# Kernel optimization log

Hardware: AMD Instinct MI355X
Metric: run time of the kernel (lower is better)

## Reference

```python
import jax, jax.numpy as jnp
import numpy as np

MAX_NORM = 1.0 - 1e-5  # Poincare ball (c=1) boundary clip, geoopt-style
NUM_HEADS = 8

def _norm(x):
    return jnp.sqrt(jnp.sum(x * x, axis=-1, keepdims=True) + 1e-30)

def projx(x):
    n = _norm(x)
    return jnp.where(n > MAX_NORM, x * (MAX_NORM / n), x)

def expmap0(u):
    n = _norm(u)
    return jnp.tanh(n) * u / n

def logmap0(x):
    n = _norm(x)
    return jnp.arctanh(jnp.minimum(n, MAX_NORM)) * x / n

def mobius_add(x, y):
    xy = jnp.sum(x * y, axis=-1, keepdims=True)
    x2 = jnp.sum(x * x, axis=-1, keepdims=True)
    y2 = jnp.sum(y * y, axis=-1, keepdims=True)
    num = (1.0 + 2.0 * xy + y2) * x + (1.0 - x2) * y
    den = 1.0 + 2.0 * xy + x2 * y2
    return num / jnp.maximum(den, 1e-15)

def mobius_matvec(M, x):
    xn = _norm(x)
    mx = x @ M.T
    mxn = _norm(mx)
    return jnp.tanh(mxn / xn * jnp.arctanh(jnp.minimum(xn, MAX_NORM))) * mx / mxn

def man_linear(x, W, b):
    # Manifold_Linear: mobius matvec + mobius bias add + project (geoopt MobiusLinear)
    return projx(mobius_add(mobius_matvec(W, x), b))

def mob_relu(x):
    # Mob_Act(ReLU): act in tangent space at origin
    return projx(expmap0(jax.nn.relu(logmap0(x))))

def layer_norm(x, g, b):
    mu = jnp.mean(x, axis=-1, keepdims=True)
    v = jnp.var(x, axis=-1, keepdims=True)
    return (x - mu) / jnp.sqrt(v + 1e-5) * g + b

def mha_tan_space(x_q, x_kv, Wq, bq, Wk, bk, Wv, bv, Wo, bo, num_heads):
    # ManifoldMHA with att_metric='tan_space': manifold linear projections,
    # scaled dot-product attention in the tangent space at the origin.
    q = logmap0(man_linear(x_q, Wq, bq))   # (S, B, E)
    k = logmap0(man_linear(x_kv, Wk, bk))  # (T, B, E)
    v = logmap0(man_linear(x_kv, Wv, bv))  # (T, B, E)
    S, B, E = q.shape
    hd = E // num_heads
    def split(t):  # (T,B,E) -> (B,H,T,hd)
        return t.reshape(t.shape[0], B, num_heads, hd).transpose(1, 2, 0, 3)
    qh, kh, vh = split(q), split(k), split(v)
    scores = jnp.einsum('bhqd,bhkd->bhqk', qh, kh) / np.sqrt(hd).astype(np.float32)
    attn = jax.nn.softmax(scores, axis=-1)
    o = jnp.einsum('bhqk,bhkd->bhqd', attn, vh)  # (B,H,S,hd)
    o = o.transpose(2, 0, 1, 3).reshape(S, B, E)
    o = expmap0(o)
    return man_linear(o, Wo, bo)

def forward_block(x, ln1_g, ln1_b, ln2_g, ln2_b, Wq, bq, Wk, bk, Wv, bv, Wo, bo, W1, b1, W2, b2):
    residual = x
    h = expmap0(layer_norm(logmap0(x), ln1_g, ln1_b))
    h = mha_tan_space(h, h, Wq, bq, Wk, bk, Wv, bv, Wo, bo, NUM_HEADS)
    h = projx(h)
    h = projx(mobius_add(h, residual))
    residual = h
    h = projx(expmap0(layer_norm(logmap0(h), ln2_g, ln2_b)))
    h = mob_relu(man_linear(h, W1, b1))   # fc1 = Manifold_Linear + Mob_Act
    h = projx(h)                          # act_dropout (identity, eval) + projx
    h = mob_relu(man_linear(h, W2, b2))   # fc2
    h = projx(mobius_add(h, residual))
    return h

def setup_inputs() -> dict:
    key = jax.random.key(0)
    ks = jax.random.split(key, 18)
    S, B, E, F = 128, 256, 512, 2048
    sE = 1.0 / np.sqrt(E)
    sF = 1.0 / np.sqrt(F)
    # input points must lie inside the unit ball: randn scaled small
    x = jax.random.normal(ks[0], (S, B, E), jnp.float32) * 0.02
    def w(k, o, i, s):
        return jax.random.normal(k, (o, i), jnp.float32) * s
    def bias(k, d):
        return jax.random.normal(k, (d,), jnp.float32) * 1e-3
    return {
        'x': x,
        'ln1_g': jnp.ones((E,), jnp.float32), 'ln1_b': jnp.zeros((E,), jnp.float32),
        'ln2_g': jnp.ones((E,), jnp.float32), 'ln2_b': jnp.zeros((E,), jnp.float32),
        'Wq': w(ks[1], E, E, sE), 'bq': bias(ks[2], E),
        'Wk': w(ks[3], E, E, sE), 'bk': bias(ks[4], E),
        'Wv': w(ks[5], E, E, sE), 'bv': bias(ks[6], E),
        'Wo': w(ks[7], E, E, sE), 'bo': bias(ks[8], E),
        'W1': w(ks[9], F, E, sE), 'b1': bias(ks[10], F),
        'W2': w(ks[11], E, F, sF), 'b2': bias(ks[12], E),
    }

def reference(x, ln1_g, ln1_b, ln2_g, ln2_b, Wq, bq, Wk, bk, Wv, bv, Wo, bo, W1, b1, W2, b2):
    return forward_block(x, ln1_g, ln1_b, ln2_g, ln2_b, Wq, bq, Wk, bk, Wv, bv, Wo, bo, W1, b1, W2, b2)
```

## Files before the change

kernel.cpp:

```cpp
#include <hip/hip_runtime.h>
#include <math.h>

#define S_DIM 128
#define B_DIM 256
#define E_DIM 512
#define F_DIM 2048
#define N_ROWS (S_DIM * B_DIM)
#define CH 8192
#define MAXN 0.99999f

typedef __bf16 bf16x8 __attribute__((ext_vector_type(8)));
typedef float f32x4 __attribute__((ext_vector_type(4)));

__device__ __forceinline__ float frcp(float x) { return __builtin_amdgcn_rcpf(x); }
__device__ __forceinline__ float frsq(float x) { return __builtin_amdgcn_rsqf(x); }
__device__ __forceinline__ float fexp2(float x) { return __builtin_amdgcn_exp2f(x); }
__device__ __forceinline__ float flog2(float x) { return __builtin_amdgcn_logf(x); }
__device__ __forceinline__ float fatanh(float x) {
  return 0.34657359f * flog2((1.f + x) * frcp(1.f - x));
}
__device__ __forceinline__ float ftanh(float x) {
  float t = fexp2(x * -2.88539008f);
  return (1.f - t) * frcp(1.f + t);
}

__device__ __forceinline__ ushort f2bf(float f) {
  __bf16 h = (__bf16)f;
  return __builtin_bit_cast(ushort, h);
}
__device__ __forceinline__ uint pack2(float a, float b) {
  return (uint)f2bf(a) | ((uint)f2bf(b) << 16);
}

__device__ __forceinline__ void gld16(const ushort* g, ushort* l) {
  __builtin_amdgcn_global_load_lds(
      (const __attribute__((address_space(1))) void*)g,
      (__attribute__((address_space(3))) void*)l, 16, 0, 0);
}

template <int K>
__device__ __forceinline__ void waveRed(float (&v)[K]) {
#pragma unroll
  for (int o = 1; o < 64; o <<= 1) {
#pragma unroll
    for (int i = 0; i < K; ++i) v[i] += __shfl_xor(v[i], o);
  }
}

__global__ __launch_bounds__(256) void k_f2bf(const float* __restrict__ in,
                                              ushort* __restrict__ out, int n) {
  for (int i = blockIdx.x * 256 + threadIdx.x; i < n; i += gridDim.x * 256)
    out[i] = f2bf(in[i]);
}

__global__ void k_bsums(const float* __restrict__ bq, const float* __restrict__ bk,
                        const float* __restrict__ bv, const float* __restrict__ g1,
                        const float* __restrict__ lb1, float* __restrict__ bs) {
  int lane = threadIdx.x;
  float p[6];
#pragma unroll
  for (int i = 0; i < 6; ++i) p[i] = 0.f;
  for (int i = lane; i < E_DIM; i += 64) {
    float a = bq[i]; p[0] += a * a;
    a = bk[i]; p[1] += a * a;
    a = bv[i]; p[2] += a * a;
    float g = g1[i], l = lb1[i];
    p[3] += g * g; p[4] += g * l; p[5] += l * l;
  }
  waveRed<6>(p);
  if (lane == 0) {
    bs[0] = p[0]; bs[1] = p[1]; bs[2] = p[2];
    bs[7] = p[3]; bs[8] = p[4]; bs[9] = p[5];
  }
}

__global__ __launch_bounds__(256) void k_stage1(
    const float* __restrict__ x, const float* __restrict__ g,
    const float* __restrict__ bb, const float* __restrict__ bs,
    ushort* __restrict__ h, float* __restrict__ hn) {
  int wv = threadIdx.x >> 6, lane = threadIdx.x & 63;
  int row = blockIdx.x * 8 + wv * 2;
  size_t base = (size_t)row * E_DIM + lane * 8;
  float v[2][8], gv[8], bv[8];
  *(float4*)&v[0][0] = *(const float4*)(x + base);
  *(float4*)&v[0][4] = *(const float4*)(x + base + 4);
  *(float4*)&v[1][0] = *(const float4*)(x + base + E_DIM);
  *(float4*)&v[1][4] = *(const float4*)(x + base + E_DIM + 4);
  *(float4*)&gv[0] = *(const float4*)(g + lane * 8);
  *(float4*)&gv[4] = *(const float4*)(g + lane * 8 + 4);
  *(float4*)&bv[0] = *(const float4*)(bb + lane * 8);
  *(float4*)&bv[4] = *(const float4*)(bb + lane * 8 + 4);
  float s[10];
#pragma unroll
  for (int i = 0; i < 10; ++i) s[i] = 0.f;
#pragma unroll
  for (int i = 0; i < 8; ++i) {
    float gg = gv[i] * gv[i], gb = gv[i] * bv[i];
#pragma unroll
    for (int r2 = 0; r2 < 2; ++r2) {
      float vv = v[r2][i];
      s[r2 * 5 + 0] += vv * vv;
      s[r2 * 5 + 1] += vv;
      s[r2 * 5 + 2] += vv * vv * gg;
      s[r2 * 5 + 3] += vv * gg;
      s[r2 * 5 + 4] += vv * gb;
    }
  }
  waveRed<10>(s);
  float Sg2 = bs[7], Sgb = bs[8], Sb2 = bs[9];
#pragma unroll
  for (int r2 = 0; r2 < 2; ++r2) {
    float T0 = s[r2 * 5 + 0], T1 = s[r2 * 5 + 1], T2 = s[r2 * 5 + 2];
    float T3 = s[r2 * 5 + 3], T4 = s[r2 * 5 + 4];
    float se = T0 + 1e-30f;
    float rn = frsq(se);
    float n = se * rn;
    float a = fatanh(fminf(n, MAXN)) * rn;
    float mu = a * T1 * (1.f / 512.f);
    float var = fmaxf(a * a * T0 * (1.f / 512.f) - mu * mu, 0.f);
    float rstd = frsq(var + 1e-5f);
    float A = a * rstd, B = -mu * rstd;
    float se2 = fmaxf(A * A * T2 + 2.f * A * B * T3 + 2.f * A * T4 +
                          B * B * Sg2 + 2.f * B * Sgb + Sb2, 0.f) + 1e-30f;
    float rn2 = frsq(se2);
    float n2 = se2 * rn2;
    float th = ftanh(n2);
    float f = th * rn2;
    float e[8];
#pragma unroll
    for (int i = 0; i < 8; ++i) e[i] = (A * v[r2][i] + B) * gv[i] + bv[i];
    uint4 o = {pack2(e[0] * f, e[1] * f), pack2(e[2] * f, e[3] * f),
               pack2(e[4] * f, e[5] * f), pack2(e[6] * f, e[7] * f)};
    *reinterpret_cast<uint4*>(h + base + r2 * E_DIM) = o;
    if (lane == 0) hn[row + r2] = th;
  }
}

__global__ __launch_bounds__(256) void k_qkv_fused(
    const ushort* __restrict__ A, const ushort* __restrict__ B,
    const float* __restrict__ xn_arr, const float* __restrict__ bias,
    const float* __restrict__ bs_sb2, ushort* __restrict__ qout) {
  __shared__ __align__(16) ushort As[32 * 32];
  __shared__ __align__(16) ushort Bs[512 * 32];
  __shared__ float redu[2][32][4];
  __shared__ float coefA[32], coefB[32];
  const int K = E_DIM;
  int tid = threadIdx.x;
  int w = tid >> 6, lane = tid & 63;
  int r0 = blockIdx.x * 32;

  const ushort* gA =
      A + ((size_t)r0 + (w & 1) * 16 + (lane >> 2)) * K + (lane & 3) * 8;
  ushort* lA = As + ((w & 1) * 16) * 32;
  const ushort* gB = B + ((size_t)w * 128 + (lane >> 2)) * K + (lane & 3) * 8;
  ushort* lB = Bs + (w * 128) * 32;

  int fro = (lane & 15) * 32 + (lane >> 4) * 8;
  const ushort* raA = As + fro;
  const ushort* raB = Bs + w * 128 * 32 + fro;

  f32x4 zero = {0.f, 0.f, 0.f, 0.f};
  f32x4 acc[2][8];
#pragma unroll
  for (int i = 0; i < 2; ++i)
#pragma unroll
    for (int j = 0; j < 8; ++j) acc[i][j] = zero;

  for (int kt = 0; kt < K; kt += 32) {
    __syncthreads();
    if (w < 2) gld16(gA + kt, lA);
#pragma unroll
    for (int i = 0; i < 8; ++i)
      gld16(gB + kt + (size_t)i * 16 * K, lB + i * 16 * 32);
    __syncthreads();
    bf16x8 af[2], bfv[8];
    af[0] = *reinterpret_cast<const bf16x8*>(raA);
    af[1] = *reinterpret_cast<const bf16x8*>(raA + 512);
#pragma unroll
    for (int j = 0; j < 8; ++j)
      bfv[j] = *reinterpret_cast<const bf16x8*>(raB + j * 512);
#pragma unroll
    for (int i = 0; i < 2; ++i)
#pragma unroll
      for (int j = 0; j < 8; ++j)
        acc[i][j] = __builtin_amdgcn_mfma_f32_16x16x32_bf16(af[i], bfv[j],
                                                            acc[i][j], 0, 0, 0);
  }

  float bvv[8];
#pragma unroll
  for (int j = 0; j < 8; ++j) bvv[j] = bias[w * 128 + j * 16 + (lane & 15)];
#pragma unroll
  for (int ti = 0; ti < 2; ++ti) {
#pragma unroll
    for (int reg = 0; reg < 4; ++reg) {
      float p2 = 0.f, pb = 0.f;
#pragma unroll
      for (int j = 0; j < 8; ++j) {
        float c = acc[ti][j][reg];
        p2 += c * c;
        pb += c * bvv[j];
      }
#pragma unroll
      for (int o = 1; o < 16; o <<= 1) {
        p2 += __shfl_xor(p2, o);
        pb += __shfl_xor(pb, o);
      }
      if ((lane & 15) == 0) {
        int row = ti * 16 + (lane >> 4) * 4 + reg;
        redu[0][row][w] = p2;
        redu[1][row][w] = pb;
      }
    }
  }
  __syncthreads();
  if (tid < 32) {
    int row = tid;
    float S0 = (redu[0][row][0] + redu[0][row][1]) +
               (redu[0][row][2] + redu[0][row][3]);
    float S1 = (redu[1][row][0] + redu[1][row][1]) +
               (redu[1][row][2] + redu[1][row][3]);
    float S2 = *bs_sb2;
    float se = S0 + 1e-30f;
    float rmx = frsq(se);
    float mxn = se * rmx;
    float xn = xn_arr[r0 + row];
    float aa = fatanh(fminf(xn, MAXN));
    float tt = ftanh(mxn * frcp(xn) * aa);
    float c = tt * rmx;
    float xy = c * S1, y2 = S2, x2 = tt * tt;
    float c1 = 1.f + 2.f * xy + y2, c2 = 1.f - x2;
    float iden = frcp(fmaxf(1.f + 2.f * xy + x2 * y2, 1e-15f));
    float cc1 = c1 * c * iden, cc2 = c2 * iden;
    float un2 =
        fmaxf(cc1 * cc1 * S0 + 2.f * cc1 * cc2 * S1 + cc2 * cc2 * S2, 0.f);
    float ue = un2 + 1e-30f;
    float run = frsq(ue);
    float un = ue * run;
    float ne = fminf(un, MAXN);
    float f = fatanh(ne) * run;
    coefA[row] = cc1 * f;
    coefB[row] = cc2 * f;
  }
  __syncthreads();
#pragma unroll
  for (int ti = 0; ti < 2; ++ti) {
#pragma unroll
    for (int reg = 0; reg < 4; ++reg) {
      int row = ti * 16 + (lane >> 4) * 4 + reg;
      float cA = coefA[row], cB = coefB[row];
      ushort* orow = qout + (size_t)(r0 + row) * E_DIM + w * 128 + (lane & 15);
#pragma unroll
      for (int j = 0; j < 8; ++j)
        orow[j * 16] = f2bf(cA * acc[ti][j][reg] + cB * bvv[j]);
    }
  }
}

__global__ __launch_bounds__(256) void k_gemm_bf16(
    const ushort* __restrict__ A, const ushort* __restrict__ B,
    float* __restrict__ C, int K, int M, int kseg,
    unsigned long long partStride) {
  __shared__ __align__(16) ushort As[128 * 32];
  __shared__ __align__(16) ushort Bs[128 * 32];
  int tid = threadIdx.x;
  int w = tid >> 6, lane = tid & 63;
  int wm = w >> 1, wn = w & 1;
  size_t row0 = (size_t)blockIdx.y * 128;
  size_t col0 = (size_t)blockIdx.x * 128;
  int k0 = blockIdx.z * kseg;

  const ushort* gA =
      A + (row0 + w * 32 + (lane >> 2)) * (size_t)K + (lane & 3) * 8 + k0;
  const ushort* gB =
      B + (col0 + w * 32 + (lane >> 2)) * (size_t)K + (lane & 3) * 8 + k0;
  ushort* lA = As + (w * 32) * 32;
  ushort* lB = Bs + (w * 32) * 32;
  const int rowK16 = 16 * K;

  int fro = (lane & 15) * 32 + (lane >> 4) * 8;
  const ushort* raA = As + (wm * 64) * 32 + fro;
  const ushort* raB = Bs + (wn * 64) * 32 + fro;

  f32x4 zero = {0.f, 0.f, 0.f, 0.f};
  f32x4 acc[4][4];
#pragma unroll
  for (int i = 0; i < 4; ++i)
#pragma unroll
    for (int j = 0; j < 4; ++j) acc[i][j] = zero;

  for (int kt = 0; kt < kseg; kt += 32) {
    __syncthreads();
    gld16(gA + kt, lA);
    gld16(gA + kt + rowK16, lA + 16 * 32);
    gld16(gB + kt, lB);
    gld16(gB + kt + rowK16, lB + 16 * 32);
    __syncthreads();
    bf16x8 af[4], bfv[4];
#pragma unroll
    for (int t = 0; t < 4; ++t) {
      af[t] = *reinterpret_cast<const bf16x8*>(raA + t * 512);
      bfv[t] = *reinterpret_cast<const bf16x8*>(raB + t * 512);
    }
#pragma unroll
    for (int i = 0; i < 4; ++i)
#pragma unroll
      for (int j = 0; j < 4; ++j)
        acc[i][j] = __builtin_amdgcn_mfma_f32_16x16x32_bf16(af[i], bfv[j],
                                                            acc[i][j], 0, 0, 0);
  }
  float* Cz = C + (size_t)blockIdx.z * partStride;
  int crow = wm * 64 + (lane >> 4) * 4;
  int ccol = (int)col0 + wn * 64 + (lane & 15);
#pragma unroll
  for (int ti = 0; ti < 4; ++ti) {
    size_t r = row0 + crow + ti * 16;
#pragma unroll
    for (int tj = 0; tj < 4; ++tj) {
      int cc = ccol + tj * 16;
#pragma unroll
      for (int reg = 0; reg < 4; ++reg)
        Cz[(r + reg) * (size_t)M + cc] = acc[ti][tj][reg];
    }
  }
}

__global__ __launch_bounds__(256) void k_attn(const ushort* __restrict__ q,
                                              const ushort* __restrict__ k,
                                              const ushort* __restrict__ v,
                                              float* __restrict__ o) {
  __shared__ __align__(16) ushort smem[27136];
  ushort* Qs = smem;
  ushort* Ks = smem + 9216;
  ushort* VTs = smem + 18432;
  ushort* Ps = smem;
  int bh = blockIdx.x;
  int b = bh >> 3, h = bh & 7;
  int tid = threadIdx.x;
  int w = tid >> 6, lane = tid & 63;
  const size_t BE = (size_t)B_DIM * E_DIM;
  size_t gbase = (size_t)b * E_DIM + (size_t)h * 64;

  {
    int s = tid >> 1, half = (tid & 1) * 32;
    const ushort* qr = q + gbase + (size_t)s * BE + half;
    const ushort* kr = k + gbase + (size_t)s * BE + half;
    const ushort* vr = v + gbase + (size_t)s * BE + half;
#pragma unroll
    for (int j = 0; j < 4; ++j) {
      *reinterpret_cast<uint4*>(&Qs[s * 72 + half + j * 8]) =
          *reinterpret_cast<const uint4*>(qr + j * 8);
      *reinterpret_cast<uint4*>(&Ks[s * 72 + half + j * 8]) =
          *reinterpret_cast<const uint4*>(kr + j * 8);
    }
    ushort tv[32];
#pragma unroll
    for (int j = 0; j < 4; ++j)
      *reinterpret_cast<uint4*>(&tv[j * 8]) =
          *reinterpret_cast<const uint4*>(vr + j * 8);
#pragma unroll
    for (int d = 0; d < 32; ++d) VTs[(half + d) * 136 + s] = tv[d];
  }
  __syncthreads();

  f32x4 zero = {0.f, 0.f, 0.f, 0.f};
  f32x4 sacc[2][8];
#pragma unroll
  for (int i = 0; i < 2; ++i)
#pragma unroll
    for (int j = 0; j < 8; ++j) sacc[i][j] = zero;
  {
    const ushort* qb = Qs + (w * 32 + (lane & 15)) * 72 + (lane >> 4) * 8;
    const ushort* kb = Ks + (lane & 15) * 72 + (lane >> 4) * 8;
#pragma unroll
    for (int kk = 0; kk < 2; ++kk) {
      bf16x8 a0 = *reinterpret_cast<const bf16x8*>(qb + kk * 32);
      bf16x8 a1 = *reinterpret_cast<const bf16x8*>(qb + 16 * 72 + kk * 32);
#pragma unroll
      for (int tj = 0; tj < 8; ++tj) {
        bf16x8 bf = *reinterpret_cast<const bf16x8*>(kb + tj * 16 * 72 + kk * 32);
        sacc[0][tj] = __builtin_amdgcn_mfma_f32_16x16x32_bf16(a0, bf,
                                                              sacc[0][tj], 0, 0, 0);
        sacc[1][tj] = __builtin_amdgcn_mfma_f32_16x16x32_bf16(a1, bf,
                                                              sacc[1][tj], 0, 0, 0);
      }
    }
  }

#pragma unroll
  for (int ti = 0; ti < 2; ++ti) {
#pragma unroll
    for (int r = 0; r < 4; ++r) {
      float mx = -1e30f;
#pragma unroll
      for (int tj = 0; tj < 8; ++tj) mx = fmaxf(mx, sacc[ti][tj][r]);
      mx = fmaxf(mx, __shfl_xor(mx, 1));
      mx = fmaxf(mx, __shfl_xor(mx, 2));
      mx = fmaxf(mx, __shfl_xor(mx, 4));
      mx = fmaxf(mx, __shfl_xor(mx, 8));
      float l = 0.f;
#pragma unroll
      for (int tj = 0; tj < 8; ++tj) {
        float e = fexp2((sacc[ti][tj][r] - mx) * (0.125f * 1.44269504f));
        sacc[ti][tj][r] = e;
        l += e;
      }
      l += __shfl_xor(l, 1);
      l += __shfl_xor(l, 2);
      l += __shfl_xor(l, 4);
      l += __shfl_xor(l, 8);
      float inv = frcp(l);
#pragma unroll
      for (int tj = 0; tj < 8; ++tj) sacc[ti][tj][r] *= inv;
    }
  }

  __syncthreads();
  {
    int qr0 = w * 32 + (lane >> 4) * 4;
    int kc = lane & 15;
#pragma unroll
    for (int ti = 0; ti < 2; ++ti)
#pragma unroll
      for (int tj = 0; tj < 8; ++tj)
#pragma unroll
        for (int r = 0; r < 4; ++r)
          Ps[(qr0 + ti * 16 + r) * 136 + tj * 16 + kc] =
              f2bf(sacc[ti][tj][r]);
  }
  __syncthreads();

  f32x4 oacc[2][4];
#pragma unroll
  for (int i = 0; i < 2; ++i)
#pragma unroll
    for (int j = 0; j < 4; ++j) oacc[i][j] = zero;
  {
    const ushort* pb = Ps + (w * 32 + (lane & 15)) * 136 + (lane >> 4) * 8;
    const ushort* vb = VTs + (lane & 15) * 136 + (lane >> 4) * 8;
#pragma unroll
    for (int kk = 0; kk < 4; ++kk) {
      bf16x8 a0 = *reinterpret_cast<const bf16x8*>(pb + kk * 32);
      bf16x8 a1 = *reinterpret_cast<const bf16x8*>(pb + 16 * 136 + kk * 32);
#pragma unroll
      for (int tj = 0; tj < 4; ++tj) {
        bf16x8 bv = *reinterpret_cast<const bf16x8*>(vb + tj * 16 * 136 + kk * 32);
        oacc[0][tj] = __builtin_amdgcn_mfma_f32_16x16x32_bf16(a0, bv,
                                                              oacc[0][tj], 0, 0, 0);
        oacc[1][tj] = __builtin_amdgcn_mfma_f32_16x16x32_bf16(a1, bv,
                                                              oacc[1][tj], 0, 0, 0);
      }
    }
  }

  {
    int qr0 = w * 32 + (lane >> 4) * 4;
    int dc = lane & 15;
#pragma unroll
    for (int ti = 0; ti < 2; ++ti)
#pragma unroll
      for (int tj = 0; tj < 4; ++tj)
#pragma unroll
        for (int r = 0; r < 4; ++r)
          o[(size_t)(qr0 + ti * 16 + r) * BE + gbase + tj * 16 + dc] =
              oacc[ti][tj][r];
  }
}

__global__ __launch_bounds__(256) void k_expmap_rows(const float* __restrict__ in,
                                                     ushort* __restrict__ out,
                                                     float* __restrict__ nrm) {
  int wv = threadIdx.x >> 6, lane = threadIdx.x & 63;
  int row = blockIdx.x * 8 + wv * 2;
  size_t base = (size_t)row * E_DIM + lane * 8;
  float v[2][8];
  *(float4*)&v[0][0] = *(const float4*)(in + base);
  *(float4*)&v[0][4] = *(const float4*)(in + base + 4);
  *(float4*)&v[1][0] = *(const float4*)(in + base + E_DIM);
  *(float4*)&v[1][4] = *(const float4*)(in + base + E_DIM + 4);
  float s[2] = {0.f, 0.f};
#pragma unroll
  for (int i = 0; i < 8; ++i) {
    s[0] += v[0][i] * v[0][i];
    s[1] += v[1][i] * v[1][i];
  }
  waveRed<2>(s);
#pragma unroll
  for (int r2 = 0; r2 < 2; ++r2) {
    float se = s[r2] + 1e-30f;
    float rn = frsq(se);
    float n = se * rn;
    float th = ftanh(n);
    float f = th * rn;
    uint4 o = {pack2(v[r2][0] * f, v[r2][1] * f), pack2(v[r2][2] * f, v[r2][3] * f),
               pack2(v[r2][4] * f, v[r2][5] * f), pack2(v[r2][6] * f, v[r2][7] * f)};
    *reinterpret_cast<uint4*>(out + base + r2 * E_DIM) = o;
    if (lane == 0) nrm[row + r2] = th;
  }
}

__global__ __launch_bounds__(256) void k_epi_attnout(
    float* __restrict__ mo, const float* __restrict__ xn_arr,
    const float* __restrict__ bo, const float* __restrict__ xin,
    const float* __restrict__ g2, const float* __restrict__ b2,
    ushort* __restrict__ h2, float* __restrict__ h2n) {
  int row = blockIdx.x * 4 + (threadIdx.x >> 6);
  int lane = threadIdx.x & 63;
  size_t base = (size_t)row * E_DIM + lane * 8;
  float m[8], bv[8];
  *(float4*)&m[0] = *(const float4*)(mo + base);
  *(float4*)&m[4] = *(const float4*)(mo + base + 4);
  *(float4*)&bv[0] = *(const float4*)(bo + lane * 8);
  *(float4*)&bv[4] = *(const float4*)(bo + lane * 8 + 4);
  float s[5] = {0.f, 0.f, 0.f, 0.f, 0.f};
#pragma unroll
  for (int i = 0; i < 8; ++i) {
    s[0] += m[i] * m[i]; s[1] += m[i] * bv[i]; s[2] += bv[i] * bv[i];
    s[3] += m[i]; s[4] += bv[i];
  }
  waveRed<5>(s);
  float se = s[0] + 1e-30f;
  float rmx = frsq(se);
  float mxn = se * rmx;
  float xn = xn_arr[row];
  float aa = fatanh(fminf(xn, MAXN));
  float tt = ftanh(mxn * frcp(xn) * aa);
  float c = tt * rmx;
  float xy = c * s[1], y2 = s[2], x2 = tt * tt;
  float c1 = 1.f + 2.f * xy + y2, c2 = 1.f - x2;
  float iden = frcp(fmaxf(1.f + 2.f * xy + x2 * y2, 1e-15f));
  float cc1 = c1 * c * iden, cc2 = c2 * iden;
  float un2 = fmaxf(cc1 * cc1 * s[0] + 2.f * cc1 * cc2 * s[1] + cc2 * cc2 * s[2], 0.f);
  float ue = un2 + 1e-30f;
  float run = frsq(ue);
  float un = ue * run;
  float ps = un > MAXN ? MAXN * run : 1.f;
  float zn = fminf(un, MAXN);
  float z[8];
#pragma unroll
  for (int i = 0; i < 8; ++i) z[i] = (cc1 * m[i] + cc2 * bv[i]) * ps;
  float sumz = ps * (cc1 * s[3] + cc2 * s[4]);
  float r[8];
  *(float4*)&r[0] = *(const float4*)(xin + base);
  *(float4*)&r[4] = *(const float4*)(xin + base + 4);
  float t2[3] = {0.f, 0.f, 0.f};
#pragma unroll
  for (int i = 0; i < 8; ++i) {
    t2[0] += z[i] * r[i]; t2[1] += r[i] * r[i]; t2[2] += r[i];
  }
  waveRed<3>(t2);
  float xy2 = t2[0], y22 = t2[1], x22 = zn * zn;
  float d1 = 1.f + 2.f * xy2 + y22, d2 = 1.f - x22;
  float iden2 = frcp(fmaxf(1.f + 2.f * xy2 + x22 * y22, 1e-15f));
  float wn2 = fmaxf(iden2 * iden2 *
                        (d1 * d1 * x22 + 2.f * d1 * d2 * xy2 + d2 * d2 * y22),
                    0.f);
  float we = wn2 + 1e-30f;
  float rwn = frsq(we);
  float wn = we * rwn;
  float ps2 = wn > MAXN ? MAXN * rwn : 1.f;
  float w[8];
#pragma unroll
  for (int i = 0; i < 8; ++i) w[i] = (d1 * z[i] + d2 * r[i]) * iden2 * ps2;
  *(float4*)(mo + base) = *(float4*)&w[0];
  *(float4*)(mo + base + 4) = *(float4*)&w[4];
  float ne = fminf(wn, MAXN);
  float ath = fatanh(ne);
  float lf = ath * frcp(ne);
  float sumw = ps2 * iden2 * (d1 * sumz + d2 * t2[2]);
  float mu = lf * sumw * (1.f / 512.f);
  float var = fmaxf(ath * ath * (1.f / 512.f) - mu * mu, 0.f);
  float rstd = frsq(var + 1e-5f);
  float gv[8], b2v[8];
  *(float4*)&gv[0] = *(const float4*)(g2 + lane * 8);
  *(float4*)&gv[4] = *(const float4*)(g2 + lane * 8 + 4);
  *(float4*)&b2v[0] = *(const float4*)(b2 + lane * 8);
  *(float4*)&b2v[4] = *(const float4*)(b2 + lane * 8 + 4);
  float e[8];
  float s3[1] = {0.f};
#pragma unroll
  for (int i = 0; i < 8; ++i) {
    e[i] = (lf * w[i] - mu) * rstd * gv[i] + b2v[i];
    s3[0] += e[i] * e[i];
  }
  waveRed<1>(s3);
  float s3e = s3[0] + 1e-30f;
  float rn3 = frsq(s3e);
  float n3 = s3e * rn3;
  float en = ftanh(n3);
  float f = en * rn3;
  if (en > MAXN) f *= MAXN * frcp(en);
  uint4 o = {pack2(e[0] * f, e[1] * f), pack2(e[2] * f, e[3] * f),
             pack2(e[4] * f, e[5] * f), pack2(e[6] * f, e[7] * f)};
  *reinterpret_cast<uint4*>(h2 + base) = o;
  if (lane == 0) h2n[row] = fminf(en, MAXN);
}

__global__ __launch_bounds__(256) void k_epi_ffn1(const float* __restrict__ mr_,
                                                  const float* __restrict__ xn_arr,
                                                  const float* __restrict__ bias,
                                                  ushort* __restrict__ hid,
                                                  float* __restrict__ hn_out) {
  int wv = threadIdx.x >> 6, lane = threadIdx.x & 63;
  int row = blockIdx.x * 8 + wv * 2;
  const float* mr = mr_ + (size_t)row * F_DIM + lane * 32;
  const float* br = bias + lane * 32;
  float m[2][32], bv[32];
#pragma unroll
  for (int j = 0; j < 8; ++j) {
    *(float4*)&m[0][j * 4] = *(const float4*)(mr + j * 4);
    *(float4*)&m[1][j * 4] = *(const float4*)(mr + F_DIM + j * 4);
    *(float4*)&bv[j * 4] = *(const float4*)(br + j * 4);
  }
  float s[5];
#pragma unroll
  for (int i = 0; i < 5; ++i) s[i] = 0.f;
#pragma unroll
  for (int i = 0; i < 32; ++i) {
#pragma unroll
    for (int r2 = 0; r2 < 2; ++r2) {
      s[r2 * 2 + 0] += m[r2][i] * m[r2][i];
      s[r2 * 2 + 1] += m[r2][i] * bv[i];
    }
    s[4] += bv[i] * bv[i];
  }
  waveRed<5>(s);
  float s2[2] = {0.f, 0.f};
#pragma unroll
  for (int r2 = 0; r2 < 2; ++r2) {
    float S0 = s[r2 * 2 + 0], S1 = s[r2 * 2 + 1], S2 = s[4];
    float se = S0 + 1e-30f;
    float rmx = frsq(se);
    float mxn = se * rmx;
    float xn = xn_arr[row + r2];
    float aa = fatanh(fminf(xn, MAXN));
    float tt = ftanh(mxn * frcp(xn) * aa);
    float c = tt * rmx;
    float xy = c * S1, y2 = S2, x2 = tt * tt;
    float c1 = 1.f + 2.f * xy + y2, c2 = 1.f - x2;
    float iden = frcp(fmaxf(1.f + 2.f * xy + x2 * y2, 1e-15f));
    float cc1 = c1 * c * iden, cc2 = c2 * iden;
    float un2 = fmaxf(cc1 * cc1 * S0 + 2.f * cc1 * cc2 * S1 + cc2 * cc2 * S2, 0.f);
    float ue = un2 + 1e-30f;
    float run = frsq(ue);
    float un = ue * run;
    float zn = fminf(un, MAXN);
    float lf = fatanh(zn) * run;
#pragma unroll
    for (int i = 0; i < 32; ++i) {
      m[r2][i] = fmaxf((cc1 * m[r2][i] + cc2 * bv[i]) * lf, 0.f);
      s2[r2] += m[r2][i] * m[r2][i];
    }
  }
  waveRed<2>(s2);
#pragma unroll
  for (int r2 = 0; r2 < 2; ++r2) {
    float s2e = s2[r2] + 1e-30f;
    float rrn = frsq(s2e);
    float rn = s2e * rrn;
    float en = ftanh(rn);
    float f = en * rrn;
    if (en > MAXN) f *= MAXN * frcp(en);
    ushort* hr = hid + (size_t)(row + r2) * F_DIM + lane * 32;
#pragma unroll
    for (int j = 0; j < 4; ++j) {
      uint4 o = {pack2(m[r2][j * 8 + 0] * f, m[r2][j * 8 + 1] * f),
                 pack2(m[r2][j * 8 + 2] * f, m[r2][j * 8 + 3] * f),
                 pack2(m[r2][j * 8 + 4] * f, m[r2][j * 8 + 5] * f),
                 pack2(m[r2][j * 8 + 6] * f, m[r2][j * 8 + 7] * f)};
      *reinterpret_cast<uint4*>(hr + j * 8) = o;
    }
    if (lane == 0) hn_out[row + r2] = fminf(en, MAXN);
  }
}

__global__ __launch_bounds__(256) void k_epi_final(
    const float* __restrict__ m2, const float* __restrict__ xn_arr,
    const float* __restrict__ bias, const float* __restrict__ res,
    float* __restrict__ out) {
  int wv = threadIdx.x >> 6, lane = threadIdx.x & 63;
  int row = blockIdx.x * 8 + wv * 2;
  size_t base = (size_t)row * E_DIM + lane * 8;
  const size_t P2 = (size_t)CH * E_DIM;
  float m[2][8], bv[8], q[2][8];
#pragma unroll
  for (int r2 = 0; r2 < 2; ++r2) {
    float ta[8], tb[8];
    *(float4*)&ta[0] = *(const float4*)(m2 + base + r2 * E_DIM);
    *(float4*)&ta[4] = *(const float4*)(m2 + base + r2 * E_DIM + 4);
    *(float4*)&tb[0] = *(const float4*)(m2 + P2 + base + r2 * E_DIM);
    *(float4*)&tb[4] = *(const float4*)(m2 + P2 + base + r2 * E_DIM + 4);
#pragma unroll
    for (int i = 0; i < 8; ++i) m[r2][i] = ta[i] + tb[i];
    *(float4*)&q[r2][0] = *(const float4*)(res + base + r2 * E_DIM);
    *(float4*)&q[r2][4] = *(const float4*)(res + base + r2 * E_DIM + 4);
  }
  *(float4*)&bv[0] = *(const float4*)(bias + lane * 8);
  *(float4*)&bv[4] = *(const float4*)(bias + lane * 8 + 4);
  float s[7];
#pragma unroll
  for (int i = 0; i < 7; ++i) s[i] = 0.f;
#pragma unroll
  for (int i = 0; i < 8; ++i) {
#pragma unroll
    for (int r2 = 0; r2 < 2; ++r2) {
      s[r2 * 3 + 0] += m[r2][i] * m[r2][i];
      s[r2 * 3 + 1] += m[r2][i] * bv[i];
      s[r2 * 3 + 2] += q[r2][i] * q[r2][i];
    }
    s[6] += bv[i] * bv[i];
  }
  waveRed<7>(s);
  float r[2][8];
  float s2[4];
#pragma unroll
  for (int i = 0; i < 4; ++i) s2[i] = 0.f;
#pragma unroll
  for (int r2 = 0; r2 < 2; ++r2) {
    float S0 = s[r2 * 3 + 0], S1 = s[r2 * 3 + 1], S2 = s[6];
    float se = S0 + 1e-30f;
    float rmx = frsq(se);
    float mxn = se * rmx;
    float xn = xn_arr[row + r2];
    float aa = fatanh(fminf(xn, MAXN));
    float tt = ftanh(mxn * frcp(xn) * aa);
    float c = tt * rmx;
    float xy = c * S1, y2 = S2, x2 = tt * tt;
    float c1 = 1.f + 2.f * xy + y2, c2 = 1.f - x2;
    float iden = frcp(fmaxf(1.f + 2.f * xy + x2 * y2, 1e-15f));
    float cc1 = c1 * c * iden, cc2 = c2 * iden;
    float un2 = fmaxf(cc1 * cc1 * S0 + 2.f * cc1 * cc2 * S1 + cc2 * cc2 * S2, 0.f);
    float ue = un2 + 1e-30f;
    float run = frsq(ue);
    float un = ue * run;
    float zn = fminf(un, MAXN);
    float lf = fatanh(zn) * run;
#pragma unroll
    for (int i = 0; i < 8; ++i) {
      r[r2][i] = fmaxf((cc1 * m[r2][i] + cc2 * bv[i]) * lf, 0.f);
      s2[r2 * 2 + 0] += r[r2][i] * r[r2][i];
      s2[r2 * 2 + 1] += r[r2][i] * q[r2][i];
    }
  }
  waveRed<4>(s2);
#pragma unroll
  for (int r2 = 0; r2 < 2; ++r2) {
    float s2e = s2[r2 * 2 + 0] + 1e-30f;
    float rrn = frsq(s2e);
    float rn = s2e * rrn;
    float en = ftanh(rn);
    float f = en * rrn;
    if (en > MAXN) f *= MAXN * frcp(en);
    float hn = fminf(en, MAXN);
    float xy2 = f * s2[r2 * 2 + 1], y22 = s[r2 * 3 + 2], x22 = hn * hn;
    float d1 = 1.f + 2.f * xy2 + y22, d2 = 1.f - x22;
    float iden2 = frcp(fmaxf(1.f + 2.f * xy2 + x22 * y22, 1e-15f));
    float wn2 = fmaxf(iden2 * iden2 *
                          (d1 * d1 * x22 + 2.f * d1 * d2 * xy2 + d2 * d2 * y22),
                      0.f);
    float we = wn2 + 1e-30f;
    float rwn = frsq(we);
    float wn = we * rwn;
    float ps2 = wn > MAXN ? MAXN * rwn : 1.f;
    float w[8];
#pragma unroll
    for (int i = 0; i < 8; ++i)
      w[i] = (d1 * r[r2][i] * f + d2 * q[r2][i]) * iden2 * ps2;
    *(float4*)(out + base + r2 * E_DIM) = *(float4*)&w[0];
    *(float4*)(out + base + r2 * E_DIM + 4) = *(float4*)&w[4];
  }
}

extern "C" void kernel_launch(void* const* d_in, const int* in_sizes, int n_in,
                              void* d_out, int out_size, void* d_ws,
                              size_t ws_size, hipStream_t stream) {
  const float* x   = (const float*)d_in[0];
  const float* g1  = (const float*)d_in[1];
  const float* lb1 = (const float*)d_in[2];
  const float* g2  = (const float*)d_in[3];
  const float* lb2 = (const float*)d_in[4];
  const float* Wq  = (const float*)d_in[5];
  const float* bq  = (const float*)d_in[6];
  const float* Wk  = (const float*)d_in[7];
  const float* bk  = (const float*)d_in[8];
  const float* Wv  = (const float*)d_in[9];
  const float* bv  = (const float*)d_in[10];
  const float* Wo  = (const float*)d_in[11];
  const float* bo  = (const float*)d_in[12];
  const float* W1  = (const float*)d_in[13];
  const float* b1  = (const float*)d_in[14];
  const float* W2  = (const float*)d_in[15];
  const float* b2  = (const float*)d_in[16];
  float* out = (float*)d_out;
  float* ws = (float*)d_ws;

  const size_t NE = (size_t)N_ROWS * E_DIM;
  const size_t WF = (4 * (size_t)E_DIM * E_DIM +
                     2 * (size_t)F_DIM * E_DIM) / 2;
  float* R_b = ws;
  float* R_a = ws + NE;
  float* R_q = ws + NE + NE / 2;
  float* R_k = ws + 2 * NE;
  float* R_v = ws + 2 * NE + NE / 2;
  ushort* wqb = (ushort*)(ws + 3 * NE);
  ushort* wkb = wqb + (size_t)E_DIM * E_DIM;
  ushort* wvb = wkb + (size_t)E_DIM * E_DIM;
  ushort* wob = wvb + (size_t)E_DIM * E_DIM;
  ushort* w1b = wob + (size_t)E_DIM * E_DIM;
  ushort* w2b = w1b + (size_t)F_DIM * E_DIM;
  float* n_h1 = ws + 3 * NE + WF;
  float* n_oe = n_h1 + N_ROWS;
  float* n_h2 = n_oe + N_ROWS;
  float* n_h3 = n_h2 + N_ROWS;
  float* bs = n_h3 + N_ROWS;
  const size_t need = (3 * NE + WF + 4 * (size_t)N_ROWS + 16) * sizeof(float);
  if (ws_size < need) return;

  k_bsums<<<1, 64, 0, stream>>>(bq, bk, bv, g1, lb1, bs);
  k_f2bf<<<256, 256, 0, stream>>>(Wq, wqb, E_DIM * E_DIM);
  k_f2bf<<<256, 256, 0, stream>>>(Wk, wkb, E_DIM * E_DIM);
  k_f2bf<<<256, 256, 0, stream>>>(Wv, wvb, E_DIM * E_DIM);
  k_f2bf<<<256, 256, 0, stream>>>(Wo, wob, E_DIM * E_DIM);
  k_f2bf<<<512, 256, 0, stream>>>(W1, w1b, F_DIM * E_DIM);
  k_f2bf<<<512, 256, 0, stream>>>(W2, w2b, F_DIM * E_DIM);

  ushort* h1b = (ushort*)R_a;
  ushort* qb = (ushort*)R_q;
  ushort* kb = (ushort*)R_k;
  ushort* vb = (ushort*)R_v;

  k_stage1<<<N_ROWS / 8, 256, 0, stream>>>(x, g1, lb1, bs, h1b, n_h1);
  k_qkv_fused<<<N_ROWS / 32, 256, 0, stream>>>(h1b, wqb, n_h1, bq, bs + 0, qb);
  k_qkv_fused<<<N_ROWS / 32, 256, 0, stream>>>(h1b, wkb, n_h1, bk, bs + 1, kb);
  k_qkv_fused<<<N_ROWS / 32, 256, 0, stream>>>(h1b, wvb, n_h1, bv, bs + 2, vb);

  k_attn<<<B_DIM * 8, 256, 0, stream>>>(qb, kb, vb, R_b);
  ushort* oeb = (ushort*)R_a;
  k_expmap_rows<<<N_ROWS / 8, 256, 0, stream>>>(R_b, oeb, n_oe);

  ushort* h2b = (ushort*)R_a;
  dim3 gQ(E_DIM / 128, N_ROWS / 128, 1);
  k_gemm_bf16<<<gQ, 256, 0, stream>>>(oeb, wob, R_b, E_DIM, E_DIM, E_DIM, 0);
  k_epi_attnout<<<N_ROWS / 4, 256, 0, stream>>>(R_b, n_oe, bo, x, g2, lb2,
                                                h2b, n_h2);

  float* m1 = R_q;
  ushort* hidb = (ushort*)R_v;
  float* m2 = R_q;
  for (int c = 0; c < N_ROWS / CH; ++c) {
    size_t ro = (size_t)c * CH;
    k_gemm_bf16<<<dim3(F_DIM / 128, CH / 128, 1), 256, 0, stream>>>(
        h2b + ro * E_DIM, w1b, m1, E_DIM, F_DIM, E_DIM, 0);
    k_epi_ffn1<<<CH / 8, 256, 0, stream>>>(m1, n_h2 + ro, b1, hidb, n_h3 + ro);
    k_gemm_bf16<<<dim3(E_DIM / 128, CH / 128, 2), 256, 0, stream>>>(
        hidb, w2b, m2, F_DIM, E_DIM, F_DIM / 2,
        (unsigned long long)((size_t)CH * E_DIM));
    k_epi_final<<<CH / 8, 256, 0, stream>>>(m2, n_h3 + ro, b2,
                                            R_b + ro * E_DIM, out + ro * E_DIM);
  }
}
```

Baseline: 873.8 us.

## Store intermediates in bf16 and split QKV into GEMM plus epilogue

Several intermediates that were kept in fp32 are now written as bf16: GEMM outputs for QKV, attention-out and FFN1, the attention output, and the residual. This halves their global memory traffic. The fused QKV kernel, which used 32-row tiles and a 512-wide B tile, is replaced by the generic 128x128 GEMM writing bf16 plus a separate epilogue kernel. That adds a round trip through memory but may give better GEMM tiling. The bf16 rounding of pre-epilogue values, including the norms computed from them, adds some precision loss.

New measurement: 844.0 us. -3.4%, faster.

```diff
diff --git a/kernel.cpp b/kernel.cpp
--- a/kernel.cpp
+++ b/kernel.cpp
@@ -30,6 +30,17 @@
 }
 __device__ __forceinline__ uint pack2(float a, float b) {
   return (uint)f2bf(a) | ((uint)f2bf(b) << 16);
+}
+__device__ __forceinline__ void ldbf8(const ushort* p, float (&f)[8]) {
+  uint4 u = *reinterpret_cast<const uint4*>(p);
+  f[0] = __uint_as_float(u.x << 16);
+  f[1] = __uint_as_float(u.x & 0xFFFF0000u);
+  f[2] = __uint_as_float(u.y << 16);
+  f[3] = __uint_as_float(u.y & 0xFFFF0000u);
+  f[4] = __uint_as_float(u.z << 16);
+  f[5] = __uint_as_float(u.z & 0xFFFF0000u);
+  f[6] = __uint_as_float(u.w << 16);
+  f[7] = __uint_as_float(u.w & 0xFFFF0000u);
 }
 
 __device__ __forceinline__ void gld16(const ushort* g, ushort* l) {
@@ -136,131 +147,10 @@
   }
 }
 
-__global__ __launch_bounds__(256) void k_qkv_fused(
-    const ushort* __restrict__ A, const ushort* __restrict__ B,
-    const float* __restrict__ xn_arr, const float* __restrict__ bias,
-    const float* __restrict__ bs_sb2, ushort* __restrict__ qout) {
-  __shared__ __align__(16) ushort As[32 * 32];
-  __shared__ __align__(16) ushort Bs[512 * 32];
-  __shared__ float redu[2][32][4];
-  __shared__ float coefA[32], coefB[32];
-  const int K = E_DIM;
-  int tid = threadIdx.x;
-  int w = tid >> 6, lane = tid & 63;
-  int r0 = blockIdx.x * 32;
-
-  const ushort* gA =
-      A + ((size_t)r0 + (w & 1) * 16 + (lane >> 2)) * K + (lane & 3) * 8;
-  ushort* lA = As + ((w & 1) * 16) * 32;
-  const ushort* gB = B + ((size_t)w * 128 + (lane >> 2)) * K + (lane & 3) * 8;
-  ushort* lB = Bs + (w * 128) * 32;
-
-  int fro = (lane & 15) * 32 + (lane >> 4) * 8;
-  const ushort* raA = As + fro;
-  const ushort* raB = Bs + w * 128 * 32 + fro;
-
-  f32x4 zero = {0.f, 0.f, 0.f, 0.f};
-  f32x4 acc[2][8];
-#pragma unroll
-  for (int i = 0; i < 2; ++i)
-#pragma unroll
-    for (int j = 0; j < 8; ++j) acc[i][j] = zero;
-
-  for (int kt = 0; kt < K; kt += 32) {
-    __syncthreads();
-    if (w < 2) gld16(gA + kt, lA);
-#pragma unroll
-    for (int i = 0; i < 8; ++i)
-      gld16(gB + kt + (size_t)i * 16 * K, lB + i * 16 * 32);
-    __syncthreads();
-    bf16x8 af[2], bfv[8];
-    af[0] = *reinterpret_cast<const bf16x8*>(raA);
-    af[1] = *reinterpret_cast<const bf16x8*>(raA + 512);
-#pragma unroll
-    for (int j = 0; j < 8; ++j)
-      bfv[j] = *reinterpret_cast<const bf16x8*>(raB + j * 512);
-#pragma unroll
-    for (int i = 0; i < 2; ++i)
-#pragma unroll
-      for (int j = 0; j < 8; ++j)
-        acc[i][j] = __builtin_amdgcn_mfma_f32_16x16x32_bf16(af[i], bfv[j],
-                                                            acc[i][j], 0, 0, 0);
-  }
-
-  float bvv[8];
-#pragma unroll
-  for (int j = 0; j < 8; ++j) bvv[j] = bias[w * 128 + j * 16 + (lane & 15)];
-#pragma unroll
-  for (int ti = 0; ti < 2; ++ti) {
-#pragma unroll
-    for (int reg = 0; reg < 4; ++reg) {
-      float p2 = 0.f, pb = 0.f;
-#pragma unroll
-      for (int j = 0; j < 8; ++j) {
-        float c = acc[ti][j][reg];
-        p2 += c * c;
-        pb += c * bvv[j];
-      }
-#pragma unroll
-      for (int o = 1; o < 16; o <<= 1) {
-        p2 += __shfl_xor(p2, o);
-        pb += __shfl_xor(pb, o);
-      }
-      if ((lane & 15) == 0) {
-        int row = ti * 16 + (lane >> 4) * 4 + reg;
-        redu[0][row][w] = p2;
-        redu[1][row][w] = pb;
-      }
-    }
-  }
-  __syncthreads();
-  if (tid < 32) {
-    int row = tid;
-    float S0 = (redu[0][row][0] + redu[0][row][1]) +
-               (redu[0][row][2] + redu[0][row][3]);
-    float S1 = (redu[1][row][0] + redu[1][row][1]) +
-               (redu[1][row][2] + redu[1][row][3]);
-    float S2 = *bs_sb2;
-    float se = S0 + 1e-30f;
-    float rmx = frsq(se);
-    float mxn = se * rmx;
-    float xn = xn_arr[r0 + row];
-    float aa = fatanh(fminf(xn, MAXN));
-    float tt = ftanh(mxn * frcp(xn) * aa);
-    float c = tt * rmx;
-    float xy = c * S1, y2 = S2, x2 = tt * tt;
-    float c1 = 1.f + 2.f * xy + y2, c2 = 1.f - x2;
-    float iden = frcp(fmaxf(1.f + 2.f * xy + x2 * y2, 1e-15f));
-    float cc1 = c1 * c * iden, cc2 = c2 * iden;
-    float un2 =
-        fmaxf(cc1 * cc1 * S0 + 2.f * cc1 * cc2 * S1 + cc2 * cc2 * S2, 0.f);
-    float ue = un2 + 1e-30f;
-    float run = frsq(ue);
-    float un = ue * run;
-    float ne = fminf(un, MAXN);
-    float f = fatanh(ne) * run;
-    coefA[row] = cc1 * f;
-    coefB[row] = cc2 * f;
-  }
-  __syncthreads();
-#pragma unroll
-  for (int ti = 0; ti < 2; ++ti) {
-#pragma unroll
-    for (int reg = 0; reg < 4; ++reg) {
-      int row = ti * 16 + (lane >> 4) * 4 + reg;
-      float cA = coefA[row], cB = coefB[row];
-      ushort* orow = qout + (size_t)(r0 + row) * E_DIM + w * 128 + (lane & 15);
-#pragma unroll
-      for (int j = 0; j < 8; ++j)
-        orow[j * 16] = f2bf(cA * acc[ti][j][reg] + cB * bvv[j]);
-    }
-  }
-}
-
 __global__ __launch_bounds__(256) void k_gemm_bf16(
     const ushort* __restrict__ A, const ushort* __restrict__ B,
     float* __restrict__ C, int K, int M, int kseg,
-    unsigned long long partStride) {
+    unsigned long long partStride, int obf) {
   __shared__ __align__(16) ushort As[128 * 32];
   __shared__ __align__(16) ushort Bs[128 * 32];
   int tid = threadIdx.x;
@@ -309,26 +199,96 @@
         acc[i][j] = __builtin_amdgcn_mfma_f32_16x16x32_bf16(af[i], bfv[j],
                                                             acc[i][j], 0, 0, 0);
   }
-  float* Cz = C + (size_t)blockIdx.z * partStride;
   int crow = wm * 64 + (lane >> 4) * 4;
   int ccol = (int)col0 + wn * 64 + (lane & 15);
-#pragma unroll
-  for (int ti = 0; ti < 4; ++ti) {
-    size_t r = row0 + crow + ti * 16;
-#pragma unroll
-    for (int tj = 0; tj < 4; ++tj) {
-      int cc = ccol + tj * 16;
-#pragma unroll
-      for (int reg = 0; reg < 4; ++reg)
-        Cz[(r + reg) * (size_t)M + cc] = acc[ti][tj][reg];
-    }
+  if (obf) {
+    ushort* Cu = (ushort*)C;
+#pragma unroll
+    for (int ti = 0; ti < 4; ++ti) {
+      size_t r = row0 + crow + ti * 16;
+#pragma unroll
+      for (int tj = 0; tj < 4; ++tj) {
+        int cc = ccol + tj * 16;
+#pragma unroll
+        for (int reg = 0; reg < 4; ++reg)
+          Cu[(r + reg) * (size_t)M + cc] = f2bf(acc[ti][tj][reg]);
+      }
+    }
+  } else {
+    float* Cz = C + (size_t)blockIdx.z * partStride;
+#pragma unroll
+    for (int ti = 0; ti < 4; ++ti) {
+      size_t r = row0 + crow + ti * 16;
+#pragma unroll
+      for (int tj = 0; tj < 4; ++tj) {
+        int cc = ccol + tj * 16;
+#pragma unroll
+        for (int reg = 0; reg < 4; ++reg)
+          Cz[(r + reg) * (size_t)M + cc] = acc[ti][tj][reg];
+      }
+    }
+  }
+}
+
+__global__ __launch_bounds__(256) void k_epi_qkv(const ushort* __restrict__ mx,
+                                                 const float* __restrict__ xn_arr,
+                                                 const float* __restrict__ bias,
+                                                 const float* __restrict__ bs_sb2,
+                                                 ushort* __restrict__ qout) {
+  int wv = threadIdx.x >> 6, lane = threadIdx.x & 63;
+  int row = blockIdx.x * 8 + wv * 2;
+  size_t base = (size_t)row * E_DIM + lane * 8;
+  float m[2][8], bv[8];
+  ldbf8(mx + base, m[0]);
+  ldbf8(mx + base + E_DIM, m[1]);
+  *(float4*)&bv[0] = *(const float4*)(bias + lane * 8);
+  *(float4*)&bv[4] = *(const float4*)(bias + lane * 8 + 4);
+  float s[4];
+#pragma unroll
+  for (int i = 0; i < 4; ++i) s[i] = 0.f;
+#pragma unroll
+  for (int i = 0; i < 8; ++i) {
+#pragma unroll
+    for (int r2 = 0; r2 < 2; ++r2) {
+      s[r2 * 2 + 0] += m[r2][i] * m[r2][i];
+      s[r2 * 2 + 1] += m[r2][i] * bv[i];
+    }
+  }
+  waveRed<4>(s);
+  float S2 = *bs_sb2;
+#pragma unroll
+  for (int r2 = 0; r2 < 2; ++r2) {
+    float S0 = s[r2 * 2 + 0], S1 = s[r2 * 2 + 1];
+    float se = S0 + 1e-30f;
+    float rmx = frsq(se);
+    float mxn = se * rmx;
+    float xn = xn_arr[row + r2];
+    float aa = fatanh(fminf(xn, MAXN));
+    float tt = ftanh(mxn * frcp(xn) * aa);
+    float c = tt * rmx;
+    float xy = c * S1, y2 = S2, x2 = tt * tt;
+    float c1 = 1.f + 2.f * xy + y2, c2 = 1.f - x2;
+    float iden = frcp(fmaxf(1.f + 2.f * xy + x2 * y2, 1e-15f));
+    float cc1 = c1 * c * iden, cc2 = c2 * iden;
+    float un2 = fmaxf(cc1 * cc1 * S0 + 2.f * cc1 * cc2 * S1 + cc2 * cc2 * S2, 0.f);
+    float ue = un2 + 1e-30f;
+    float run = frsq(ue);
+    float un = ue * run;
+    float ne = fminf(un, MAXN);
+    float f = fatanh(ne) * run;
+    float u[8];
+#pragma unroll
+    for (int i = 0; i < 8; ++i) u[i] = (cc1 * m[r2][i] + cc2 * bv[i]) * f;
+    uint4 o = {pack2(u[0], u[1]), pack2(u[2], u[3]), pack2(u[4], u[5]),
+               pack2(u[6], u[7])};
+    *reinterpret_cast<uint4*>(qout + base + r2 * E_DIM) = o;
   }
 }
 
 __global__ __launch_bounds__(256) void k_attn(const ushort* __restrict__ q,
                                               const ushort* __restrict__ k,
                                               const ushort* __restrict__ v,
-                                              float* __restrict__ o) {
+                                              ushort* __restrict__ o) {
   __shared__ __align__(16) ushort smem[27136];
   ushort* Qs = smem;
   ushort* Ks = smem + 9216;
@@ -463,21 +423,19 @@
 #pragma unroll
         for (int r = 0; r < 4; ++r)
           o[(size_t)(qr0 + ti * 16 + r) * BE + gbase + tj * 16 + dc] =
-              oacc[ti][tj][r];
-  }
-}
-
-__global__ __launch_bounds__(256) void k_expmap_rows(const float* __restrict__ in,
+              f2bf(oacc[ti][tj][r]);
+  }
+}
+
+__global__ __launch_bounds__(256) void k_expmap_rows(const ushort* __restrict__ in,
                                                      ushort* __restrict__ out,
                                                      float* __restrict__ nrm) {
   int wv = threadIdx.x >> 6, lane = threadIdx.x & 63;
   int row = blockIdx.x * 8 + wv * 2;
   size_t base = (size_t)row * E_DIM + lane * 8;
   float v[2][8];
-  *(float4*)&v[0][0] = *(const float4*)(in + base);
-  *(float4*)&v[0][4] = *(const float4*)(in + base + 4);
-  *(float4*)&v[1][0] = *(const float4*)(in + base + E_DIM);
-  *(float4*)&v[1][4] = *(const float4*)(in + base + E_DIM + 4);
+  ldbf8(in + base, v[0]);
+  ldbf8(in + base + E_DIM, v[1]);
   float s[2] = {0.f, 0.f};
 #pragma unroll
   for (int i = 0; i < 8; ++i) {
@@ -500,16 +458,16 @@
 }
 
 __global__ __launch_bounds__(256) void k_epi_attnout(
-    float* __restrict__ mo, const float* __restrict__ xn_arr,
+    const ushort* __restrict__ mo, const float* __restrict__ xn_arr,
     const float* __restrict__ bo, const float* __restrict__ xin,
     const float* __restrict__ g2, const float* __restrict__ b2,
-    ushort* __restrict__ h2, float* __restrict__ h2n) {
+    ushort* __restrict__ h2, float* __restrict__ h2n,
+    ushort* __restrict__ r2o) {
   int row = blockIdx.x * 4 + (threadIdx.x >> 6);
   int lane = threadIdx.x & 63;
   size_t base = (size_t)row * E_DIM + lane * 8;
   float m[8], bv[8];
-  *(float4*)&m[0] = *(const float4*)(mo + base);
-  *(float4*)&m[4] = *(const float4*)(mo + base + 4);
+  ldbf8(mo + base, m);
   *(float4*)&bv[0] = *(const float4*)(bo + lane * 8);
   *(float4*)&bv[4] = *(const float4*)(bo + lane * 8 + 4);
   float s[5] = {0.f, 0.f, 0.f, 0.f, 0.f};
@@ -562,8 +520,9 @@
   float w[8];
 #pragma unroll
   for (int i = 0; i < 8; ++i) w[i] = (d1 * z[i] + d2 * r[i]) * iden2 * ps2;
-  *(float4*)(mo + base) = *(float4*)&w[0];
-  *(float4*)(mo + base + 4) = *(float4*)&w[4];
+  uint4 ro = {pack2(w[0], w[1]), pack2(w[2], w[3]), pack2(w[4], w[5]),
+              pack2(w[6], w[7])};
+  *reinterpret_cast<uint4*>(r2o + base) = ro;
   float ne = fminf(wn, MAXN);
   float ath = fatanh(ne);
   float lf = ath * frcp(ne);
@@ -596,22 +555,24 @@
   if (lane == 0) h2n[row] = fminf(en, MAXN);
 }
 
-__global__ __launch_bounds__(256) void k_epi_ffn1(const float* __restrict__ mr_,
+__global__ __launch_bounds__(256) void k_epi_ffn1(const ushort* __restrict__ mr_,
                                                   const float* __restrict__ xn_arr,
                                                   const float* __restrict__ bias,
                                                   ushort* __restrict__ hid,
                                                   float* __restrict__ hn_out) {
   int wv = threadIdx.x >> 6, lane = threadIdx.x & 63;
   int row = blockIdx.x * 8 + wv * 2;
-  const float* mr = mr_ + (size_t)row * F_DIM + lane * 32;
+  const ushort* mr = mr_ + (size_t)row * F_DIM + lane * 32;
   const float* br = bias + lane * 32;
   float m[2][32], bv[32];
 #pragma unroll
-  for (int j = 0; j < 8; ++j) {
-    *(float4*)&m[0][j * 4] = *(const float4*)(mr + j * 4);
-    *(float4*)&m[1][j * 4] = *(const float4*)(mr + F_DIM + j * 4);
+  for (int j = 0; j < 4; ++j) {
+    ldbf8(mr + j * 8, *(float(*)[8])&m[0][j * 8]);
+    ldbf8(mr + F_DIM + j * 8, *(float(*)[8])&m[1][j * 8]);
+  }
+#pragma unroll
+  for (int j = 0; j < 8; ++j)
     *(float4*)&bv[j * 4] = *(const float4*)(br + j * 4);
-  }
   float s[5];
 #pragma unroll
   for (int i = 0; i < 5; ++i) s[i] = 0.f;
@@ -676,7 +637,7 @@
 
 __global__ __launch_bounds__(256) void k_epi_final(
     const float* __restrict__ m2, const float* __restrict__ xn_arr,
-    const float* __restrict__ bias, const float* __restrict__ res,
+    const float* __restrict__ bias, const ushort* __restrict__ res,
     float* __restrict__ out) {
   int wv = threadIdx.x >> 6, lane = threadIdx.x & 63;
   int row = blockIdx.x * 8 + wv * 2;
@@ -692,8 +653,7 @@
     *(float4*)&tb[4] = *(const float4*)(m2 + P2 + base + r2 * E_DIM + 4);
 #pragma unroll
     for (int i = 0; i < 8; ++i) m[r2][i] = ta[i] + tb[i];
-    *(float4*)&q[r2][0] = *(const float4*)(res + base + r2 * E_DIM);
-    *(float4*)&q[r2][4] = *(const float4*)(res + base + r2 * E_DIM + 4);
+    ldbf8(res + base + r2 * E_DIM, q[r2]);
   }
   *(float4*)&bv[0] = *(const float4*)(bias + lane * 8);
   *(float4*)&bv[4] = *(const float4*)(bias + lane * 8 + 4);
@@ -798,6 +758,8 @@
   const size_t WF = (4 * (size_t)E_DIM * E_DIM +
                      2 * (size_t)F_DIM * E_DIM) / 2;
   float* R_b = ws;
+  ushort* Cb   = (ushort*)ws;
+  ushort* r2u  = (ushort*)(ws + NE / 2);
   float* R_a = ws + NE;
   float* R_q = ws + NE + NE / 2;
   float* R_k = ws + 2 * NE;
@@ -830,32 +792,39 @@
   ushort* vb = (ushort*)R_v;
 
   k_stage1<<<N_ROWS / 8, 256, 0, stream>>>(x, g1, lb1, bs, h1b, n_h1);
-  k_qkv_fused<<<N_ROWS / 32, 256, 0, stream>>>(h1b, wqb, n_h1, bq, bs + 0, qb);
-  k_qkv_fused<<<N_ROWS / 32, 256, 0, stream>>>(h1b, wkb, n_h1, bk, bs + 1, kb);
-  k_qkv_fused<<<N_ROWS / 32, 256, 0, stream>>>(h1b, wvb, n_h1, bv, bs + 2, vb);
-
-  k_attn<<<B_DIM * 8, 256, 0, stream>>>(qb, kb, vb, R_b);
+  dim3 gQ(E_DIM / 128, N_ROWS / 128, 1);
+  k_gemm_bf16<<<gQ, 256, 0, stream>>>(h1b, wqb, (float*)Cb, E_DIM, E_DIM,
+                                      E_DIM, 0, 1);
+  k_epi_qkv<<<N_ROWS / 8, 256, 0, stream>>>(Cb, n_h1, bq, bs + 0, qb);
+  k_gemm_bf16<<<gQ, 256, 0, stream>>>(h1b, wkb, (float*)Cb, E_DIM, E_DIM,
+                                      E_DIM, 0, 1);
+  k_epi_qkv<<<N_ROWS / 8, 256, 0, stream>>>(Cb, n_h1, bk, bs + 1, kb);
+  k_gemm_bf16<<<gQ, 256, 0, stream>>>(h1b, wvb, (float*)Cb, E_DIM, E_DIM,
+                                      E_DIM, 0, 1);
+  k_epi_qkv<<<N_ROWS / 8, 256, 0, stream>>>(Cb, n_h1, bv, bs + 2, vb);
+
+  k_attn<<<B_DIM * 8, 256, 0, stream>>>(qb, kb, vb, Cb);
   ushort* oeb = (ushort*)R_a;
-  k_expmap_rows<<<N_ROWS / 8, 256, 0, stream>>>(R_b, oeb, n_oe);
+  k_expmap_rows<<<N_ROWS / 8, 256, 0, stream>>>(Cb, oeb, n_oe);
 
   ushort* h2b = (ushort*)R_a;
-  dim3 gQ(E_DIM / 128, N_ROWS / 128, 1);
-  k_gemm_bf16<<<gQ, 256, 0, stream>>>(oeb, wob, R_b, E_DIM, E_DIM, E_DIM, 0);
-  k_epi_attnout<<<N_ROWS / 4, 256, 0, stream>>>(R_b, n_oe, bo, x, g2, lb2,
-                                                h2b, n_h2);
-
-  float* m1 = R_q;
+  k_gemm_bf16<<<gQ, 256, 0, stream>>>(oeb, wob, (float*)Cb, E_DIM, E_DIM,
+                                      E_DIM, 0, 1);
+  k_epi_attnout<<<N_ROWS / 4, 256, 0, stream>>>(Cb, n_oe, bo, x, g2, lb2,
+                                                h2b, n_h2, r2u);
+
+  ushort* m1 = Cb;
   ushort* hidb = (ushort*)R_v;
   float* m2 = R_q;
   for (int c = 0; c < N_ROWS / CH; ++c) {
     size_t ro = (size_t)c * CH;
     k_gemm_bf16<<<dim3(F_DIM / 128, CH / 128, 1), 256, 0, stream>>>(
-        h2b + ro * E_DIM, w1b, m1, E_DIM, F_DIM, E_DIM, 0);
+        h2b + ro * E_DIM, w1b, (float*)m1, E_DIM, F_DIM, E_DIM, 0, 1);
     k_epi_ffn1<<<CH / 8, 256, 0, stream>>>(m1, n_h2 + ro, b1, hidb, n_h3 + ro);
     k_gemm_bf16<<<dim3(E_DIM / 128, CH / 128, 2), 256, 0, stream>>>(
         hidb, w2b, m2, F_DIM, E_DIM, F_DIM / 2,
-        (unsigned long long)((size_t)CH * E_DIM));
+        (unsigned long long)((size_t)CH * E_DIM), 0);
     k_epi_final<<<CH / 8, 256, 0, stream>>>(m2, n_h3 + ro, b2,
-                                            R_b + ro * E_DIM, out + ro * E_DIM);
-  }
-}
+                                            r2u + ro * E_DIM, out + ro * E_DIM);
+  }
+}
```
